# Performance work log

Hardware: AMD Instinct MI355X
Metric: run time of the kernel (lower is better)

Reference implementation:

```python
import jax, jax.numpy as jnp
import numpy as np

EMB = 32  # DGM_c.input_dim

def setup_inputs() -> dict:
    key = jax.random.key(0)
    k1, k2, k3 = jax.random.split(key, 3)
    G, n, F = 32, 1024, 128
    N = G * n
    x = jax.random.normal(k1, (N, F), dtype=jnp.float32)
    W = jax.random.normal(k2, (F, EMB), dtype=jnp.float32) / np.sqrt(F)
    temperature = jnp.float32(1.0)   # nn.Parameter init 1.0
    threshold = jnp.float32(0.5)     # nn.Parameter init 0.5
    batch = jnp.repeat(jnp.arange(G, dtype=jnp.int32), n)  # equal-sized graphs
    edge_index = jax.random.randint(k3, (2, 262144), 0, N, dtype=jnp.int32)
    return {"x": x, "W": W, "temperature": temperature, "threshold": threshold,
            "batch": batch, "edge_index": edge_index, "num_graphs": G}


def reference(x, W, temperature, threshold, batch, edge_index, num_graphs):
    # x: [N, F]; equal-sized graphs of n nodes each (batch is sorted, contiguous)
    N = x.shape[0]
    G = num_graphs
    n = N // G

    # embed_f: linear projection to EMB dims (edge structure unused by this embed_f)
    xe = x @ W                                  # [N, EMB]

    # scale<0 branch fires only for the FIRST graph; centroid/scale are detached
    x0 = xe[:n]                                 # graph 0 embedding
    centroid = jax.lax.stop_gradient(jnp.mean(x0, axis=0))             # [EMB]
    scale = jax.lax.stop_gradient(0.9 / jnp.max(jnp.abs(x0 - centroid)))

    xg = ((xe - centroid) * scale).reshape(G, n, EMB)

    # squared pairwise euclidean distances per graph (cdist**2, clamped >= 0)
    sq = jnp.sum(xg * xg, axis=-1)              # [G, n]
    D = jnp.maximum(sq[:, :, None] + sq[:, None, :]
                    - 2.0 * jnp.einsum('gnd,gmd->gnm', xg, xg), 0.0)   # [G, n, n]

    A = jax.nn.sigmoid(temperature * (jnp.abs(threshold) - D))         # [G, n, n]

    # sigmoid > 0 everywhere => dense_to_sparse keeps every entry, row-major,
    # with per-graph node offsets added back.
    edge_weight = A.reshape(-1)                 # [G*n*n]
    ii = jnp.arange(n, dtype=jnp.int32)
    gi = jnp.broadcast_to(ii[:, None], (n, n)).reshape(-1)  # row index
    gj = jnp.broadcast_to(ii[None, :], (n, n)).reshape(-1)  # col index
    off = (jnp.arange(G, dtype=jnp.int32) * n)[:, None]     # [G, 1]
    src = (off + gi[None, :]).reshape(-1)
    dst = (off + gj[None, :]).reshape(-1)
    edge_index_out = jnp.stack([src, dst])      # [2, G*n*n]

    return xe, edge_index_out, edge_weight
```

## Files before the change

### kernel.cpp

```cpp
#include <hip/hip_runtime.h>

#define FDIM 128
#define EMB 32

typedef __attribute__((ext_vector_type(4))) float f32x4;
typedef __fp16 h2 __attribute__((ext_vector_type(2)));

static __device__ __forceinline__ void store_nt(float* p, float4 v) {
    f32x4 w; w.x = v.x; w.y = v.y; w.z = v.z; w.w = v.w;
    __builtin_nontemporal_store(w, (f32x4*)p);
}

static __device__ __forceinline__ unsigned pkh2(float x, float y) {
    h2 h = __builtin_amdgcn_cvt_pkrtz(x, y);
    union { h2 h; unsigned u; } c; c.h = h; return c.u;
}

static __device__ __forceinline__ float fdot2u(unsigned a, unsigned b, float c) {
    union { unsigned u; h2 h; } ua, ub; ua.u = a; ub.u = b;
#if __has_builtin(__builtin_amdgcn_fdot2)
    return __builtin_amdgcn_fdot2(ua.h, ub.h, c, false);
#else
    return c + (float)ua.h.x * (float)ub.h.x + (float)ua.h.y * (float)ub.h.y;
#endif
}

__global__ __launch_bounds__(256) void k_gemm(const float* __restrict__ x,
                                              const float* __restrict__ Wm,
                                              float* __restrict__ xe) {
    __shared__ float sW[FDIM * EMB];
    const int t = threadIdx.x;
#pragma unroll
    for (int i = 0; i < (FDIM * EMB) / (256 * 4); ++i) {
        int idx = (t + i * 256) * 4;
        *(float4*)(sW + idx) = *(const float4*)(Wm + idx);
    }
    __syncthreads();

    const int r0 = blockIdx.x * 128 + (t >> 3) * 4;
    const int e0 = (t & 7) * 4;

    float acc[4][4];
#pragma unroll
    for (int i = 0; i < 4; ++i)
#pragma unroll
        for (int j = 0; j < 4; ++j) acc[i][j] = 0.f;

    for (int k = 0; k < FDIM; k += 4) {
        float4 w0 = *(const float4*)(sW + (k + 0) * EMB + e0);
        float4 w1 = *(const float4*)(sW + (k + 1) * EMB + e0);
        float4 w2 = *(const float4*)(sW + (k + 2) * EMB + e0);
        float4 w3 = *(const float4*)(sW + (k + 3) * EMB + e0);
#pragma unroll
        for (int rr = 0; rr < 4; ++rr) {
            float4 xq = *(const float4*)(x + (size_t)(r0 + rr) * FDIM + k);
            acc[rr][0] += xq.x * w0.x + xq.y * w1.x + xq.z * w2.x + xq.w * w3.x;
            acc[rr][1] += xq.x * w0.y + xq.y * w1.y + xq.z * w2.y + xq.w * w3.y;
            acc[rr][2] += xq.x * w0.z + xq.y * w1.z + xq.z * w2.z + xq.w * w3.z;
            acc[rr][3] += xq.x * w0.w + xq.y * w1.w + xq.z * w2.w + xq.w * w3.w;
        }
    }

#pragma unroll
    for (int rr = 0; rr < 4; ++rr) {
        const size_t r = (size_t)(r0 + rr);
        float4 o; o.x = acc[rr][0]; o.y = acc[rr][1]; o.z = acc[rr][2]; o.w = acc[rr][3];
        *(float4*)(xe + r * EMB + e0) = o;
    }
}

__global__ __launch_bounds__(256) void k_stats_a(const float* __restrict__ xe,
                                                 float* __restrict__ psum,
                                                 float* __restrict__ pmin,
                                                 float* __restrict__ pmax) {
    __shared__ float rs[256], rmn[256], rmx[256];
    const int t = threadIdx.x;
    const int d = t & 31, rg = t >> 5;
    const int r0 = blockIdx.x * 32;

    float s = 0.f, mn = 3.4e38f, mx = -3.4e38f;
#pragma unroll
    for (int it = 0; it < 4; ++it) {
        float v = xe[(size_t)(r0 + rg + it * 8) * EMB + d];
        s += v; mn = fminf(mn, v); mx = fmaxf(mx, v);
    }
    rs[t] = s; rmn[t] = mn; rmx[t] = mx;
    __syncthreads();
#pragma unroll
    for (int st = 128; st >= 32; st >>= 1) {
        if (t < st) {
            rs[t] += rs[t + st];
            rmn[t] = fminf(rmn[t], rmn[t + st]);
            rmx[t] = fmaxf(rmx[t], rmx[t + st]);
        }
        __syncthreads();
    }
    if (t < 32) {
        psum[blockIdx.x * 32 + t] = rs[t];
        pmin[blockIdx.x * 32 + t] = rmn[t];
        pmax[blockIdx.x * 32 + t] = rmx[t];
    }
}

__global__ __launch_bounds__(64) void k_stats_b(const float* __restrict__ psum,
                                                const float* __restrict__ pmin,
                                                const float* __restrict__ pmax,
                                                int nb, int n,
                                                float* __restrict__ stats) {
    const int t = threadIdx.x;
    const int d = t & 31;
    float s = 0.f, mn = 3.4e38f, mx = -3.4e38f;
    for (int b = 0; b < nb; ++b) {
        s += psum[b * 32 + d];
        mn = fminf(mn, pmin[b * 32 + d]);
        mx = fmaxf(mx, pmax[b * 32 + d]);
    }
    const float c = s / (float)n;
    float dev = fmaxf(mx - c, c - mn);
#pragma unroll
    for (int off = 16; off >= 1; off >>= 1)
        dev = fmaxf(dev, __shfl_xor(dev, off, 32));
    if (t < 32) stats[t] = c;
    if (t == 0) stats[EMB] = 0.9f / dev;
}

#define DPS 68
__global__ __launch_bounds__(256) void k_edges(const float* __restrict__ xe,
                                               const float* __restrict__ stats,
                                               const float* __restrict__ tptr,
                                               const float* __restrict__ thptr,
                                               float* __restrict__ wts,
                                               float* __restrict__ srcp,
                                               float* __restrict__ dstp,
                                               int n) {
    __shared__ unsigned shA[16 * DPS];
    __shared__ unsigned shB[16 * DPS];
    __shared__ __attribute__((aligned(16))) float sqA[64];
    __shared__ __attribute__((aligned(16))) float sqB[64];

    const int g = blockIdx.z;
    const int i0 = blockIdx.y * 64, j0 = blockIdx.x * 64;
    const int t = threadIdx.x;
    const float scale = stats[EMB];

    const float* baseA = xe + ((size_t)g * n + i0) * EMB;
    const float* baseB = xe + ((size_t)g * n + j0) * EMB;

#pragma unroll
    for (int c = 0; c < 2; ++c) {
        int id = t + c * 256;
        int row = id >> 3;
        int dc = (id & 7) * 4;
        int dp = dc >> 1;
        float4 cen = *(const float4*)(stats + dc);
        float4 va = *(const float4*)(baseA + (size_t)row * EMB + dc);
        float4 vb = *(const float4*)(baseB + (size_t)row * EMB + dc);
        va.x = (va.x - cen.x) * scale; va.y = (va.y - cen.y) * scale;
        va.z = (va.z - cen.z) * scale; va.w = (va.w - cen.w) * scale;
        vb.x = (vb.x - cen.x) * scale; vb.y = (vb.y - cen.y) * scale;
        vb.z = (vb.z - cen.z) * scale; vb.w = (vb.w - cen.w) * scale;
        shA[dp * DPS + row]       = pkh2(va.x, va.y);
        shA[(dp + 1) * DPS + row] = pkh2(va.z, va.w);
        shB[dp * DPS + row]       = pkh2(vb.x, vb.y);
        shB[(dp + 1) * DPS + row] = pkh2(vb.z, vb.w);
        float pa = va.x * va.x + va.y * va.y + va.z * va.z + va.w * va.w;
        float pb = vb.x * vb.x + vb.y * vb.y + vb.z * vb.z + vb.w * vb.w;
        pa += __shfl_xor(pa, 1); pb += __shfl_xor(pb, 1);
        pa += __shfl_xor(pa, 2); pb += __shfl_xor(pb, 2);
        pa += __shfl_xor(pa, 4); pb += __shfl_xor(pb, 4);
        if ((t & 7) == 0) { sqA[row] = pa; sqB[row] = pb; }
    }
    __syncthreads();

    const int ti = t >> 4, tj = t & 15;
    float acc[4][4];
#pragma unroll
    for (int i = 0; i < 4; ++i)
#pragma unroll
        for (int j = 0; j < 4; ++j) acc[i][j] = 0.f;

#pragma unroll
    for (int dp = 0; dp < 16; ++dp) {
        uint4 ua = *(const uint4*)(shA + dp * DPS + ti * 4);
        uint4 ub = *(const uint4*)(shB + dp * DPS + tj * 4);
        unsigned av[4] = { ua.x, ua.y, ua.z, ua.w };
        unsigned bv[4] = { ub.x, ub.y, ub.z, ub.w };
#pragma unroll
        for (int u = 0; u < 4; ++u)
#pragma unroll
            for (int v = 0; v < 4; ++v)
                acc[u][v] = fdot2u(av[u], bv[v], acc[u][v]);
    }

    const float T = *tptr;
    const float TH = fabsf(*thptr);
    const int gn = g * n;
    const size_t gbase = (size_t)g * n * n;

    const float4 sq4 = *(const float4*)(sqB + tj * 4);
    const float dbase = (float)(gn + j0 + tj * 4);
    float4 dst4; dst4.x = dbase; dst4.y = dbase + 1.f; dst4.z = dbase + 2.f; dst4.w = dbase + 3.f;

#pragma unroll
    for (int u = 0; u < 4; ++u) {
        const int row = i0 + ti * 4 + u;
        const float sa = sqA[ti * 4 + u];
        const size_t off = gbase + (size_t)row * n + j0 + tj * 4;

        float4 w;
        {
            float D0 = fmaxf(sa + sq4.x - 2.f * acc[u][0], 0.f);
            float D1 = fmaxf(sa + sq4.y - 2.f * acc[u][1], 0.f);
            float D2 = fmaxf(sa + sq4.z - 2.f * acc[u][2], 0.f);
            float D3 = fmaxf(sa + sq4.w - 2.f * acc[u][3], 0.f);
            w.x = __builtin_amdgcn_rcpf(1.f + __expf(-(T * (TH - D0))));
            w.y = __builtin_amdgcn_rcpf(1.f + __expf(-(T * (TH - D1))));
            w.z = __builtin_amdgcn_rcpf(1.f + __expf(-(T * (TH - D2))));
            w.w = __builtin_amdgcn_rcpf(1.f + __expf(-(T * (TH - D3))));
        }
        store_nt(wts + off, w);

        const float sv = (float)(gn + row);
        float4 s4; s4.x = sv; s4.y = sv; s4.z = sv; s4.w = sv;
        store_nt(srcp + off, s4);
        store_nt(dstp + off, dst4);
    }
}

extern "C" void kernel_launch(void* const* d_in, const int* in_sizes, int n_in,
                              void* d_out, int out_size, void* d_ws, size_t ws_size,
                              hipStream_t stream) {
    const float* x     = (const float*)d_in[0];
    const float* Wm    = (const float*)d_in[1];
    const float* tptr  = (const float*)d_in[2];
    const float* thptr = (const float*)d_in[3];

    const int N = in_sizes[0] / FDIM;
    const long long rem = (long long)out_size - (long long)N * EMB;
    int G = (rem > 0) ? (int)((3LL * N * N) / rem) : 32;
    if (G <= 0) G = 32;
    const int n = N / G;
    const int nb = n / 32;

    float* out  = (float*)d_out;
    float* xe   = out;
    const long long M = (long long)G * n * n;
    float* srcp = out + (size_t)N * EMB;
    float* dstp = srcp + (size_t)M;
    float* wts  = dstp + (size_t)M;

    float* stats = (float*)d_ws;
    float* psum  = stats + 64;
    float* pmin  = psum + (size_t)nb * 32;
    float* pmax  = pmin + (size_t)nb * 32;

    k_gemm<<<N / 128, 256, 0, stream>>>(x, Wm, xe);
    k_stats_a<<<nb, 256, 0, stream>>>(xe, psum, pmin, pmax);
    k_stats_b<<<1, 64, 0, stream>>>(psum, pmin, pmax, nb, n, stats);
    dim3 ge(n / 64, n / 64, G);
    k_edges<<<ge, 256, 0, stream>>>(xe, stats, tptr, thptr, wts, srcp, dstp, n);
}
```

Before: 108.3 us.

## Widen edge tiles to 64x256 with fp32 swizzled LDS and full-row stores

The edge kernel now computes a 64x256 tile per block instead of 64x64. Each wavefront owns 16 rows and each lane 4 consecutive columns, so every store instruction writes a full contiguous 1 KB row segment. The packed fp16 dot2 path is replaced by fp32 FMAs from XOR-swizzled shared memory, which removes the half-precision rounding but costs more ALU work and more registers (64 accumulators). The kernel is dominated by writing about 400 MB of output, so the wider, more coalesced stores are the intended gain, and occupancy may drop in exchange.

```diff
diff --git a/kernel.cpp b/kernel.cpp
--- a/kernel.cpp
+++ b/kernel.cpp
@@ -4,25 +4,10 @@
 #define EMB 32
 
 typedef __attribute__((ext_vector_type(4))) float f32x4;
-typedef __fp16 h2 __attribute__((ext_vector_type(2)));
 
 static __device__ __forceinline__ void store_nt(float* p, float4 v) {
     f32x4 w; w.x = v.x; w.y = v.y; w.z = v.z; w.w = v.w;
     __builtin_nontemporal_store(w, (f32x4*)p);
-}
-
-static __device__ __forceinline__ unsigned pkh2(float x, float y) {
-    h2 h = __builtin_amdgcn_cvt_pkrtz(x, y);
-    union { h2 h; unsigned u; } c; c.h = h; return c.u;
-}
-
-static __device__ __forceinline__ float fdot2u(unsigned a, unsigned b, float c) {
-    union { unsigned u; h2 h; } ua, ub; ua.u = a; ub.u = b;
-#if __has_builtin(__builtin_amdgcn_fdot2)
-    return __builtin_amdgcn_fdot2(ua.h, ub.h, c, false);
-#else
-    return c + (float)ua.h.x * (float)ub.h.x + (float)ua.h.y * (float)ub.h.y;
-#endif
 }
 
 __global__ __launch_bounds__(256) void k_gemm(const float* __restrict__ x,
@@ -124,72 +109,75 @@
     if (t == 0) stats[EMB] = 0.9f / dev;
 }
 
-#define DPS 68
-__global__ __launch_bounds__(256) void k_edges(const float* __restrict__ xe,
-                                               const float* __restrict__ stats,
-                                               const float* __restrict__ tptr,
-                                               const float* __restrict__ thptr,
-                                               float* __restrict__ wts,
-                                               float* __restrict__ srcp,
-                                               float* __restrict__ dstp,
-                                               int n) {
-    __shared__ unsigned shA[16 * DPS];
-    __shared__ unsigned shB[16 * DPS];
-    __shared__ __attribute__((aligned(16))) float sqA[64];
-    __shared__ __attribute__((aligned(16))) float sqB[64];
+#define KEY(r) ((((r) >> 2) & 7) << 2)
+__global__ __launch_bounds__(256) void k_edges_w(const float* __restrict__ xe,
+                                                 const float* __restrict__ stats,
+                                                 const float* __restrict__ tptr,
+                                                 const float* __restrict__ thptr,
+                                                 float* __restrict__ wts,
+                                                 float* __restrict__ srcp,
+                                                 float* __restrict__ dstp,
+                                                 int n) {
+    __shared__ float shA[64 * 32];
+    __shared__ float shB[256 * 32];
+    __shared__ float sqA[64];
+    __shared__ __attribute__((aligned(16))) float sqB[256];
 
     const int g = blockIdx.z;
-    const int i0 = blockIdx.y * 64, j0 = blockIdx.x * 64;
+    const int i0 = blockIdx.y * 64;
+    const int j0 = blockIdx.x * 256;
     const int t = threadIdx.x;
     const float scale = stats[EMB];
-
-    const float* baseA = xe + ((size_t)g * n + i0) * EMB;
-    const float* baseB = xe + ((size_t)g * n + j0) * EMB;
-
-#pragma unroll
-    for (int c = 0; c < 2; ++c) {
+    const float* gx = xe + (size_t)g * n * EMB;
+
+#pragma unroll
+    for (int c = 0; c < 10; ++c) {
         int id = t + c * 256;
-        int row = id >> 3;
-        int dc = (id & 7) * 4;
-        int dp = dc >> 1;
+        int isB = (id >= 512);
+        int lid = isB ? (id - 512) : id;
+        int row = lid >> 3;
+        int dc = (lid & 7) * 4;
+        int grow = (isB ? j0 : i0) + row;
         float4 cen = *(const float4*)(stats + dc);
-        float4 va = *(const float4*)(baseA + (size_t)row * EMB + dc);
-        float4 vb = *(const float4*)(baseB + (size_t)row * EMB + dc);
-        va.x = (va.x - cen.x) * scale; va.y = (va.y - cen.y) * scale;
-        va.z = (va.z - cen.z) * scale; va.w = (va.w - cen.w) * scale;
-        vb.x = (vb.x - cen.x) * scale; vb.y = (vb.y - cen.y) * scale;
-        vb.z = (vb.z - cen.z) * scale; vb.w = (vb.w - cen.w) * scale;
-        shA[dp * DPS + row]       = pkh2(va.x, va.y);
-        shA[(dp + 1) * DPS + row] = pkh2(va.z, va.w);
-        shB[dp * DPS + row]       = pkh2(vb.x, vb.y);
-        shB[(dp + 1) * DPS + row] = pkh2(vb.z, vb.w);
-        float pa = va.x * va.x + va.y * va.y + va.z * va.z + va.w * va.w;
-        float pb = vb.x * vb.x + vb.y * vb.y + vb.z * vb.z + vb.w * vb.w;
-        pa += __shfl_xor(pa, 1); pb += __shfl_xor(pb, 1);
-        pa += __shfl_xor(pa, 2); pb += __shfl_xor(pb, 2);
-        pa += __shfl_xor(pa, 4); pb += __shfl_xor(pb, 4);
-        if ((t & 7) == 0) { sqA[row] = pa; sqB[row] = pb; }
+        float4 v = *(const float4*)(gx + (size_t)grow * EMB + dc);
+        v.x = (v.x - cen.x) * scale; v.y = (v.y - cen.y) * scale;
+        v.z = (v.z - cen.z) * scale; v.w = (v.w - cen.w) * scale;
+        float* sh = isB ? shB : shA;
+        *(float4*)(sh + row * 32 + (dc ^ KEY(row))) = v;
+        float ps = v.x * v.x + v.y * v.y + v.z * v.z + v.w * v.w;
+        ps += __shfl_xor(ps, 1);
+        ps += __shfl_xor(ps, 2);
+        ps += __shfl_xor(ps, 4);
+        if ((t & 7) == 0) { if (isB) sqB[row] = ps; else sqA[row] = ps; }
     }
     __syncthreads();
 
-    const int ti = t >> 4, tj = t & 15;
-    float acc[4][4];
-#pragma unroll
-    for (int i = 0; i < 4; ++i)
+    const int w = t >> 6;
+    const int l = t & 63;
+    const int keyb = (l & 7) << 2;
+    const int brow = l * 4 * 32;
+
+    float acc[16][4];
+#pragma unroll
+    for (int i = 0; i < 16; ++i)
 #pragma unroll
         for (int j = 0; j < 4; ++j) acc[i][j] = 0.f;
 
-#pragma unroll
-    for (int dp = 0; dp < 16; ++dp) {
-        uint4 ua = *(const uint4*)(shA + dp * DPS + ti * 4);
-        uint4 ub = *(const uint4*)(shB + dp * DPS + tj * 4);
-        unsigned av[4] = { ua.x, ua.y, ua.z, ua.w };
-        unsigned bv[4] = { ub.x, ub.y, ub.z, ub.w };
-#pragma unroll
-        for (int u = 0; u < 4; ++u)
-#pragma unroll
-            for (int v = 0; v < 4; ++v)
-                acc[u][v] = fdot2u(av[u], bv[v], acc[u][v]);
+    for (int d = 0; d < EMB; d += 4) {
+        const int db = d ^ keyb;
+        float4 b0 = *(const float4*)(shB + brow + 0 * 32 + db);
+        float4 b1 = *(const float4*)(shB + brow + 1 * 32 + db);
+        float4 b2 = *(const float4*)(shB + brow + 2 * 32 + db);
+        float4 b3 = *(const float4*)(shB + brow + 3 * 32 + db);
+#pragma unroll
+        for (int u = 0; u < 16; ++u) {
+            const int ar = w * 16 + u;
+            float4 a = *(const float4*)(shA + ar * 32 + (d ^ KEY(ar)));
+            acc[u][0] += a.x * b0.x + a.y * b0.y + a.z * b0.z + a.w * b0.w;
+            acc[u][1] += a.x * b1.x + a.y * b1.y + a.z * b1.z + a.w * b1.w;
+            acc[u][2] += a.x * b2.x + a.y * b2.y + a.z * b2.z + a.w * b2.w;
+            acc[u][3] += a.x * b3.x + a.y * b3.y + a.z * b3.z + a.w * b3.w;
+        }
     }
 
     const float T = *tptr;
@@ -197,28 +185,28 @@
     const int gn = g * n;
     const size_t gbase = (size_t)g * n * n;
 
-    const float4 sq4 = *(const float4*)(sqB + tj * 4);
-    const float dbase = (float)(gn + j0 + tj * 4);
+    const float4 sq4 = *(const float4*)(sqB + l * 4);
+    const float dbase = (float)(gn + j0 + l * 4);
     float4 dst4; dst4.x = dbase; dst4.y = dbase + 1.f; dst4.z = dbase + 2.f; dst4.w = dbase + 3.f;
 
 #pragma unroll
-    for (int u = 0; u < 4; ++u) {
-        const int row = i0 + ti * 4 + u;
-        const float sa = sqA[ti * 4 + u];
-        const size_t off = gbase + (size_t)row * n + j0 + tj * 4;
-
-        float4 w;
+    for (int u = 0; u < 16; ++u) {
+        const int row = i0 + w * 16 + u;
+        const float sa = sqA[w * 16 + u];
+        const size_t off = gbase + (size_t)row * n + j0 + l * 4;
+
+        float4 o;
         {
             float D0 = fmaxf(sa + sq4.x - 2.f * acc[u][0], 0.f);
             float D1 = fmaxf(sa + sq4.y - 2.f * acc[u][1], 0.f);
             float D2 = fmaxf(sa + sq4.z - 2.f * acc[u][2], 0.f);
             float D3 = fmaxf(sa + sq4.w - 2.f * acc[u][3], 0.f);
-            w.x = __builtin_amdgcn_rcpf(1.f + __expf(-(T * (TH - D0))));
-            w.y = __builtin_amdgcn_rcpf(1.f + __expf(-(T * (TH - D1))));
-            w.z = __builtin_amdgcn_rcpf(1.f + __expf(-(T * (TH - D2))));
-            w.w = __builtin_amdgcn_rcpf(1.f + __expf(-(T * (TH - D3))));
-        }
-        store_nt(wts + off, w);
+            o.x = __builtin_amdgcn_rcpf(1.f + __expf(-(T * (TH - D0))));
+            o.y = __builtin_amdgcn_rcpf(1.f + __expf(-(T * (TH - D1))));
+            o.z = __builtin_amdgcn_rcpf(1.f + __expf(-(T * (TH - D2))));
+            o.w = __builtin_amdgcn_rcpf(1.f + __expf(-(T * (TH - D3))));
+        }
+        store_nt(wts + off, o);
 
         const float sv = (float)(gn + row);
         float4 s4; s4.x = sv; s4.y = sv; s4.z = sv; s4.w = sv;
@@ -257,6 +245,6 @@
     k_gemm<<<N / 128, 256, 0, stream>>>(x, Wm, xe);
     k_stats_a<<<nb, 256, 0, stream>>>(xe, psum, pmin, pmax);
     k_stats_b<<<1, 64, 0, stream>>>(psum, pmin, pmax, nb, n, stats);
-    dim3 ge(n / 64, n / 64, G);
-    k_edges<<<ge, 256, 0, stream>>>(xe, stats, tptr, thptr, wts, srcp, dstp, n);
-}
+    dim3 ge(n / 256, n / 64, G);
+    k_edges_w<<<ge, 256, 0, stream>>>(xe, stats, tptr, thptr, wts, srcp, dstp, n);
+}
```

New measurement: 131.9 us. +21.8%, slower.
